# Performance work log

Measured on AMD Instinct MI355X. Metric: run time of the kernel, lower is better.

Reference implementation:

```python
import jax, jax.numpy as jnp
import numpy as np

N_ENTITY = 100000
N_RELATION = 32
DIM = 64
N_LAYER = 2
B = 4096
T = 32


def _knowledge_attention(h_set, path, t_emb, W1, W2):
    # h_set, path, t_emb: [B, T, D]
    x = jnp.concatenate([h_set, path], axis=-1)          # [B, T, 2D]
    a = jax.nn.sigmoid(jax.nn.sigmoid(x @ W1) @ W2)      # [B, T]
    w = jax.nn.softmax(a, axis=-1)                       # softmax over triples
    return jnp.einsum('bt,btd->bd', w, t_emb)            # [B, D]


def _branch(h_idx, r_idx, t_idx, ent, rel, W1, W2):
    # h_idx/r_idx/t_idx: [L, B, T] ints. Faithful to the original loop,
    # which re-adds layer-i head emb and re-multiplies layer-i relation emb i times.
    outs = []
    for i in range(N_LAYER):
        h_set = ent[h_idx[0]]                            # [B, T, D]
        path = rel[r_idx[0]]                             # [B, T, D]
        for _k in range(1, i + 1):
            h_set = h_set + ent[h_idx[i]]
            path = path * rel[r_idx[i]]
        outs.append(_knowledge_attention(h_set, path, ent[t_idx[i]], W1, W2))
    return outs


def setup_inputs() -> dict:
    key = jax.random.key(0)
    ks = jax.random.split(key, 20)
    d = {}
    d['items'] = jax.random.randint(ks[0], (B,), 0, N_ENTITY)
    names = ['uis', 'ipt', 'upt', 'iot']
    i = 1
    for nm in names:
        d[nm + '_h'] = jax.random.randint(ks[i], (N_LAYER, B, T), 0, N_ENTITY); i += 1
        d[nm + '_r'] = jax.random.randint(ks[i], (N_LAYER, B, T), 0, N_RELATION); i += 1
        d[nm + '_t'] = jax.random.randint(ks[i], (N_LAYER, B, T), 0, N_ENTITY); i += 1
    # xavier-ish scales
    d['ent_emb'] = jax.random.normal(ks[13], (N_ENTITY, DIM), jnp.float32) * 0.05
    d['rel_emb'] = jax.random.normal(ks[14], (N_RELATION, DIM), jnp.float32) * 0.05
    d['W1'] = jax.random.normal(ks[15], (2 * DIM, DIM), jnp.float32) * (1.0 / np.sqrt(2 * DIM))
    d['W2'] = jax.random.normal(ks[16], (DIM,), jnp.float32) * (1.0 / np.sqrt(DIM))
    return d


def reference(items, uis_h, uis_r, uis_t, ipt_h, ipt_r, ipt_t,
              upt_h, upt_r, upt_t, iot_h, iot_r, iot_t,
              ent_emb, rel_emb, W1, W2):
    # user embeddings (init triple set)
    user_embs = [ent_emb[uis_h[0]].mean(axis=1)]
    user_embs += _branch(uis_h, uis_r, uis_t, ent_emb, rel_emb, W1, W2)
    # item embeddings (potential triple set)
    item_embs = [ent_emb[items]]
    item_embs += _branch(ipt_h, ipt_r, ipt_t, ent_emb, rel_emb, W1, W2)
    # user potential embeddings
    upo_embs = [ent_emb[upt_h[0]].mean(axis=1)]
    upo_embs += _branch(upt_h, upt_r, upt_t, ent_emb, rel_emb, W1, W2)
    # item origin embeddings
    ior_embs = [ent_emb[iot_h[0]].mean(axis=1)]
    ior_embs += _branch(iot_h, iot_r, iot_t, ent_emb, rel_emb, W1, W2)
    # agg == 'sum': extra item term appended before predict
    item_embs.append(ent_emb[ipt_h[0]].mean(axis=1))
    e_u = sum(user_embs[1:], user_embs[0])
    e_i = sum(item_embs[1:], item_embs[0])
    e_p_u = sum(upo_embs[1:], upo_embs[0])
    e_p_i = sum(ior_embs[1:], ior_embs[0])
    e_u = jnp.concatenate([e_u, e_p_u], axis=-1)
    e_i = jnp.concatenate([e_p_i, e_i], axis=-1)
    scores = jax.nn.sigmoid((e_i * e_u).sum(axis=1))     # [B]
    kge_loss = jnp.float32(0.0)                          # agg='sum' path: no SSL loss
    return scores, kge_loss
```

## Files before the change

kernel.cpp:

```cpp
#include <hip/hip_runtime.h>


#define NE   100000
#define NR   32
#define DIMD 64
#define BB   4096
#define TT   32
#define BT   (BB * TT)

__device__ __forceinline__ float sigf(float x) { return 1.0f / (1.0f + __expf(-x)); }
__device__ __forceinline__ float4 ld4(const float* p) {
    return *reinterpret_cast<const float4*>(p);
}

__device__ __forceinline__ float b2f(unsigned short u) {
    return __builtin_bit_cast(float, ((unsigned)u) << 16);
}
__device__ __forceinline__ unsigned short f2b(float x) {
    unsigned b = __builtin_bit_cast(unsigned, x);
    b += 0x7FFF + ((b >> 16) & 1);
    return (unsigned short)(b >> 16);
}
__device__ __forceinline__ float4 u2f4(ushort4 v) {
    return make_float4(b2f(v.x), b2f(v.y), b2f(v.z), b2f(v.w));
}
__device__ __forceinline__ ushort4 ldu4(const unsigned short* p) {
    return *reinterpret_cast<const ushort4*>(p);
}

template <int CTRL>
__device__ __forceinline__ float dpp_add(float x) {
    int r = __builtin_amdgcn_update_dpp(0, __builtin_bit_cast(int, x), CTRL,
                                        0xf, 0xf, true);
    return x + __builtin_bit_cast(float, r);
}
__device__ __forceinline__ float reduce16(float x) {
    x = dpp_add<0x121>(x);
    x = dpp_add<0x122>(x);
    x = dpp_add<0x124>(x);
    x = dpp_add<0x128>(x);
    return x;
}

__global__ __launch_bounds__(256) void k_proj_ent(const float* __restrict__ ent,
                                                  const float* __restrict__ W1,
                                                  unsigned short* __restrict__ tab) {
    __shared__ float sR[64][68];
    const int tid = threadIdx.x;
    const int row0 = blockIdx.x * 64;

#pragma unroll
    for (int i = 0; i < 4; ++i) {
        const int idx = tid + 256 * i;
        const int r = idx >> 4;
        const int c = idx & 15;
        const int er = (row0 + r < NE) ? (row0 + r) : (NE - 1);
        const float4 rv = ld4(ent + er * DIMD + 4 * c);
        sR[r][4 * c + 0] = rv.x; sR[r][4 * c + 1] = rv.y;
        sR[r][4 * c + 2] = rv.z; sR[r][4 * c + 3] = rv.w;
    }
    __syncthreads();

    const int q = tid & 15;
    const int trow = tid >> 4;
    float4 acc0 = make_float4(0.f, 0.f, 0.f, 0.f);
    float4 acc1 = acc0, acc2 = acc0, acc3 = acc0;

#pragma unroll
    for (int kk = 0; kk < 16; ++kk) {
        const float4 r0 = ld4(&sR[4 * trow + 0][4 * kk]);
        const float4 r1 = ld4(&sR[4 * trow + 1][4 * kk]);
        const float4 r2 = ld4(&sR[4 * trow + 2][4 * kk]);
        const float4 r3 = ld4(&sR[4 * trow + 3][4 * kk]);
#pragma unroll
        for (int i = 0; i < 4; ++i) {
            const float4 wv = ld4(W1 + (4 * kk + i) * DIMD + 4 * q);
            const float s0 = (i == 0) ? r0.x : (i == 1) ? r0.y : (i == 2) ? r0.z : r0.w;
            const float s1 = (i == 0) ? r1.x : (i == 1) ? r1.y : (i == 2) ? r1.z : r1.w;
            const float s2 = (i == 0) ? r2.x : (i == 1) ? r2.y : (i == 2) ? r2.z : r2.w;
            const float s3 = (i == 0) ? r3.x : (i == 1) ? r3.y : (i == 2) ? r3.z : r3.w;
            acc0.x = fmaf(s0, wv.x, acc0.x); acc0.y = fmaf(s0, wv.y, acc0.y);
            acc0.z = fmaf(s0, wv.z, acc0.z); acc0.w = fmaf(s0, wv.w, acc0.w);
            acc1.x = fmaf(s1, wv.x, acc1.x); acc1.y = fmaf(s1, wv.y, acc1.y);
            acc1.z = fmaf(s1, wv.z, acc1.z); acc1.w = fmaf(s1, wv.w, acc1.w);
            acc2.x = fmaf(s2, wv.x, acc2.x); acc2.y = fmaf(s2, wv.y, acc2.y);
            acc2.z = fmaf(s2, wv.z, acc2.z); acc2.w = fmaf(s2, wv.w, acc2.w);
            acc3.x = fmaf(s3, wv.x, acc3.x); acc3.y = fmaf(s3, wv.y, acc3.y);
            acc3.z = fmaf(s3, wv.z, acc3.z); acc3.w = fmaf(s3, wv.w, acc3.w);
        }
    }

    const int orow = row0 + 4 * trow;
#pragma unroll
    for (int i = 0; i < 4; ++i) {
        if (orow + i < NE) {
            const float4 a = (i == 0) ? acc0 : (i == 1) ? acc1 : (i == 2) ? acc2 : acc3;
            unsigned short* rowp = tab + ((size_t)(orow + i) << 7);
            ushort4 ev, pv;
            ev.x = f2b(sR[4 * trow + i][4 * q + 0]);
            ev.y = f2b(sR[4 * trow + i][4 * q + 1]);
            ev.z = f2b(sR[4 * trow + i][4 * q + 2]);
            ev.w = f2b(sR[4 * trow + i][4 * q + 3]);
            pv.x = f2b(a.x); pv.y = f2b(a.y); pv.z = f2b(a.z); pv.w = f2b(a.w);
            *reinterpret_cast<ushort4*>(rowp + 4 * q) = ev;
            *reinterpret_cast<ushort4*>(rowp + 64 + 4 * q) = pv;
        }
    }
}

__global__ __launch_bounds__(256) void k_proj_rel(const float* __restrict__ rel,
                                                  const float* __restrict__ W1,
                                                  unsigned short* __restrict__ relB) {
    int gid = blockIdx.x * 256 + threadIdx.x;
    int row = gid >> 6;
    int d = gid & 63;
    if (row < 32) {
        const float* a = rel + row * DIMD;
        float acc = 0.0f;
#pragma unroll
        for (int k = 0; k < DIMD; ++k)
            acc = fmaf(a[k], W1[(DIMD + k) * DIMD + d], acc);
        relB[row * DIMD + d] = f2b(acc);
    } else if (row < 32 + 1024) {
        const int rr = row - 32;
        const float* a = rel + (rr >> 5) * DIMD;
        const float* c = rel + (rr & 31) * DIMD;
        float acc = 0.0f;
#pragma unroll
        for (int k = 0; k < DIMD; ++k)
            acc = fmaf(a[k] * c[k], W1[(DIMD + k) * DIMD + d], acc);
        relB[row * DIMD + d] = f2b(acc);
    }
}

__global__ __launch_bounds__(256) void k_main(
    const int* __restrict__ items,
    const int* __restrict__ uh, const int* __restrict__ ur, const int* __restrict__ ut,
    const int* __restrict__ ih, const int* __restrict__ ir, const int* __restrict__ itp,
    const int* __restrict__ ph, const int* __restrict__ pr, const int* __restrict__ pt,
    const int* __restrict__ oh, const int* __restrict__ orr, const int* __restrict__ ot,
    const unsigned short* __restrict__ tab,
    const unsigned short* __restrict__ relB,
    const float* __restrict__ W2,
    float* __restrict__ out) {
    const int b = blockIdx.x;
    const int tid = threadIdx.x;
    const int w = tid >> 6;
    const int lane = tid & 63;
    const int g = lane >> 4;
    const int q = lane & 15;

    const int* hp;
    const int* rp;
    const int* tp;
    switch (w) {
        case 0: hp = uh; rp = ur; tp = ut; break;
        case 1: hp = ih; rp = ir; tp = itp; break;
        case 2: hp = ph; rp = pr; tp = pt; break;
        default: hp = oh; rp = orr; tp = ot; break;
    }

    __shared__ int sidx[4][3][2][TT];
    {
        const int l = lane >> 5;
        const int t0 = lane & 31;
        const int off = l * BT + b * TT + t0;
        sidx[w][0][l][t0] = hp[off];
        sidx[w][1][l][t0] = rp[off];
        sidx[w][2][l][t0] = tp[off];
    }
    const int item_idx = (w == 1) ? items[b] : 0;

    int jh0[8], jh1[8], jr0[8], jr1[8], jt0[8], jt1[8];
#pragma unroll
    for (int p = 0; p < 8; ++p) {
        const int t = 4 * p + g;
        jh0[p] = sidx[w][0][0][t];
        jh1[p] = sidx[w][0][1][t];
        jr0[p] = sidx[w][1][0][t];
        jr1[p] = sidx[w][1][1][t];
        jt0[p] = sidx[w][2][0][t];
        jt1[p] = sidx[w][2][1][t];
    }

    ushort4 rH[8], rA0[8], rA1[8], rR0[8], rR2[8];
#pragma unroll
    for (int p = 0; p < 8; ++p) {
        const unsigned short* r0p = tab + ((size_t)jh0[p] << 7) + 4 * q;
        rH[p] = ldu4(r0p);
        rA0[p] = ldu4(r0p + 64);
        rA1[p] = ldu4(tab + ((size_t)jh1[p] << 7) + 64 + 4 * q);
        rR0[p] = ldu4(relB + ((size_t)jr0[p] << 6) + 4 * q);
        rR2[p] = ldu4(relB + ((size_t)(32 + jr0[p] * 32 + jr1[p]) << 6) + 4 * q);
    }

    const float4 w2v = ld4(W2 + 4 * q);

    float d0[8], d1[8];
    float4 accH = make_float4(0.f, 0.f, 0.f, 0.f);
#pragma unroll
    for (int p = 0; p < 8; ++p) {
        const float4 H = u2f4(rH[p]);
        const float4 A0 = u2f4(rA0[p]);
        const float4 A1 = u2f4(rA1[p]);
        const float4 R0 = u2f4(rR0[p]);
        const float4 R2 = u2f4(rR2[p]);

        accH.x += H.x; accH.y += H.y; accH.z += H.z; accH.w += H.w;

        float v = sigf(A0.x + R0.x) * w2v.x;
        v = fmaf(sigf(A0.y + R0.y), w2v.y, v);
        v = fmaf(sigf(A0.z + R0.z), w2v.z, v);
        v = fmaf(sigf(A0.w + R0.w), w2v.w, v);
        d0[p] = v;

        float u = sigf(A0.x + A1.x + R2.x) * w2v.x;
        u = fmaf(sigf(A0.y + A1.y + R2.y), w2v.y, u);
        u = fmaf(sigf(A0.z + A1.z + R2.z), w2v.z, u);
        u = fmaf(sigf(A0.w + A1.w + R2.w), w2v.w, u);
        d1[p] = u;
    }

    ushort4 rT0[8], rT1[8];
#pragma unroll
    for (int p = 0; p < 8; ++p) {
        rT0[p] = ldu4(tab + ((size_t)jt0[p] << 7) + 4 * q);
        rT1[p] = ldu4(tab + ((size_t)jt1[p] << 7) + 4 * q);
    }
    const ushort4 rIt = ldu4(tab + ((size_t)item_idx << 7) + 4 * q);

    float e0[8], e1[8];
    float s0 = 0.0f, s1 = 0.0f;
#pragma unroll
    for (int p = 0; p < 8; ++p) {
        e0[p] = __expf(sigf(reduce16(d0[p])));
        e1[p] = __expf(sigf(reduce16(d1[p])));
        s0 += e0[p];
        s1 += e1[p];
    }
    s0 += __shfl_xor(s0, 16, 64);
    s0 += __shfl_xor(s0, 32, 64);
    s1 += __shfl_xor(s1, 16, 64);
    s1 += __shfl_xor(s1, 32, 64);

    float4 acc0 = make_float4(0.f, 0.f, 0.f, 0.f);
    float4 acc1 = acc0;
#pragma unroll
    for (int p = 0; p < 8; ++p) {
        const float4 T0 = u2f4(rT0[p]);
        const float4 T1 = u2f4(rT1[p]);
        acc0.x = fmaf(e0[p], T0.x, acc0.x); acc0.y = fmaf(e0[p], T0.y, acc0.y);
        acc0.z = fmaf(e0[p], T0.z, acc0.z); acc0.w = fmaf(e0[p], T0.w, acc0.w);
        acc1.x = fmaf(e1[p], T1.x, acc1.x); acc1.y = fmaf(e1[p], T1.y, acc1.y);
        acc1.z = fmaf(e1[p], T1.z, acc1.z); acc1.w = fmaf(e1[p], T1.w, acc1.w);
    }

    const float inv0 = 1.0f / s0;
    const float inv1 = 1.0f / s1;
    float4 v;
    v.x = fmaf(acc0.x, inv0, fmaf(acc1.x, inv1, 0.03125f * accH.x));
    v.y = fmaf(acc0.y, inv0, fmaf(acc1.y, inv1, 0.03125f * accH.y));
    v.z = fmaf(acc0.z, inv0, fmaf(acc1.z, inv1, 0.03125f * accH.z));
    v.w = fmaf(acc0.w, inv0, fmaf(acc1.w, inv1, 0.03125f * accH.w));

    v.x += __shfl_xor(v.x, 16, 64); v.x += __shfl_xor(v.x, 32, 64);
    v.y += __shfl_xor(v.y, 16, 64); v.y += __shfl_xor(v.y, 32, 64);
    v.z += __shfl_xor(v.z, 16, 64); v.z += __shfl_xor(v.z, 32, 64);
    v.w += __shfl_xor(v.w, 16, 64); v.w += __shfl_xor(v.w, 32, 64);

    if (w == 1) {
        const float4 iv = u2f4(rIt);
        v.x += iv.x; v.y += iv.y; v.z += iv.z; v.w += iv.w;
    }

    __shared__ float vec[4][DIMD];
    if (g == 0) {
        vec[w][4 * q + 0] = v.x;
        vec[w][4 * q + 1] = v.y;
        vec[w][4 * q + 2] = v.z;
        vec[w][4 * q + 3] = v.w;
    }
    __syncthreads();

    if (tid < 64) {
        float z = fmaf(vec[0][tid], vec[3][tid], vec[2][tid] * vec[1][tid]);
#pragma unroll
        for (int m = 1; m < 64; m <<= 1) z += __shfl_xor(z, m, 64);
        if (tid == 0) out[b] = sigf(z);
    }
    if (b == 0 && tid == 0) out[BB] = 0.0f;
}

extern "C" void kernel_launch(void* const* d_in, const int* in_sizes, int n_in,
                              void* d_out, int out_size, void* d_ws, size_t ws_size,
                              hipStream_t stream) {
    const int* items = (const int*)d_in[0];
    const int* uh = (const int*)d_in[1];
    const int* ur = (const int*)d_in[2];
    const int* ut = (const int*)d_in[3];
    const int* ih = (const int*)d_in[4];
    const int* ir = (const int*)d_in[5];
    const int* itp = (const int*)d_in[6];
    const int* ph = (const int*)d_in[7];
    const int* pr = (const int*)d_in[8];
    const int* pt = (const int*)d_in[9];
    const int* oh = (const int*)d_in[10];
    const int* orr = (const int*)d_in[11];
    const int* ot = (const int*)d_in[12];
    const float* ent = (const float*)d_in[13];
    const float* rel = (const float*)d_in[14];
    const float* W1 = (const float*)d_in[15];
    const float* W2 = (const float*)d_in[16];
    float* out = (float*)d_out;

    unsigned short* relB = (unsigned short*)d_ws;
    unsigned short* tab = relB + 1056 * DIMD;

    hipLaunchKernelGGL(k_proj_ent, dim3((NE + 63) / 64), dim3(256), 0, stream,
                       ent, W1, tab);
    hipLaunchKernelGGL(k_proj_rel, dim3((1056 * 64 + 255) / 256), dim3(256), 0,
                       stream, rel, W1, relB);
    hipLaunchKernelGGL(k_main, dim3(BB), dim3(256), 0, stream, items, uh, ur, ut,
                       ih, ir, itp, ph, pr, pt, oh, orr, ot, tab, relB, W2, out);
}
```

Baseline: 202.4 us.

## Widen bf16 gathers to 16-byte loads with 8 lanes per row; stage W1 in LDS

The main kernel now assigns 8 lanes per embedding row instead of 16, so each lane gathers 8 bf16 values with one 16-byte load. It unpacks them with shift and mask, and each wave handles 8 triples per pass over 4 passes instead of 4 triples over 8. The per-triple reductions use 3 shuffle steps instead of 4 DPP steps, and the cross-group reductions gain one extra shuffle. Separately, the entity projection kernel stages W1 in shared memory instead of reading it from global memory inside the inner loop. This reduces load instruction count and gather transactions, but raises register pressure from the wider per-lane arrays.

```diff
diff --git a/kernel.cpp b/kernel.cpp
--- a/kernel.cpp
+++ b/kernel.cpp
@@ -13,38 +13,38 @@
     return *reinterpret_cast<const float4*>(p);
 }
 
-__device__ __forceinline__ float b2f(unsigned short u) {
-    return __builtin_bit_cast(float, ((unsigned)u) << 16);
-}
 __device__ __forceinline__ unsigned short f2b(float x) {
     unsigned b = __builtin_bit_cast(unsigned, x);
     b += 0x7FFF + ((b >> 16) & 1);
     return (unsigned short)(b >> 16);
 }
-__device__ __forceinline__ float4 u2f4(ushort4 v) {
-    return make_float4(b2f(v.x), b2f(v.y), b2f(v.z), b2f(v.w));
-}
-__device__ __forceinline__ ushort4 ldu4(const unsigned short* p) {
-    return *reinterpret_cast<const ushort4*>(p);
-}
-
-template <int CTRL>
-__device__ __forceinline__ float dpp_add(float x) {
-    int r = __builtin_amdgcn_update_dpp(0, __builtin_bit_cast(int, x), CTRL,
-                                        0xf, 0xf, true);
-    return x + __builtin_bit_cast(float, r);
-}
-__device__ __forceinline__ float reduce16(float x) {
-    x = dpp_add<0x121>(x);
-    x = dpp_add<0x122>(x);
-    x = dpp_add<0x124>(x);
-    x = dpp_add<0x128>(x);
+__device__ __forceinline__ float blo(unsigned u) {
+    return __builtin_bit_cast(float, u << 16);
+}
+__device__ __forceinline__ float bhi(unsigned u) {
+    return __builtin_bit_cast(float, u & 0xFFFF0000u);
+}
+__device__ __forceinline__ void unp8(uint4 v, float* f) {
+    f[0] = blo(v.x); f[1] = bhi(v.x);
+    f[2] = blo(v.y); f[3] = bhi(v.y);
+    f[4] = blo(v.z); f[5] = bhi(v.z);
+    f[6] = blo(v.w); f[7] = bhi(v.w);
+}
+__device__ __forceinline__ uint4 ldu4(const unsigned* p) {
+    return *reinterpret_cast<const uint4*>(p);
+}
+
+__device__ __forceinline__ float reduce8(float x) {
+    x += __shfl_xor(x, 1, 64);
+    x += __shfl_xor(x, 2, 64);
+    x += __shfl_xor(x, 4, 64);
     return x;
 }
 
 __global__ __launch_bounds__(256) void k_proj_ent(const float* __restrict__ ent,
                                                   const float* __restrict__ W1,
                                                   unsigned short* __restrict__ tab) {
+    __shared__ float sW[64][68];
     __shared__ float sR[64][68];
     const int tid = threadIdx.x;
     const int row0 = blockIdx.x * 64;
@@ -54,6 +54,9 @@
         const int idx = tid + 256 * i;
         const int r = idx >> 4;
         const int c = idx & 15;
+        const float4 wv = ld4(W1 + r * DIMD + 4 * c);
+        sW[r][4 * c + 0] = wv.x; sW[r][4 * c + 1] = wv.y;
+        sW[r][4 * c + 2] = wv.z; sW[r][4 * c + 3] = wv.w;
         const int er = (row0 + r < NE) ? (row0 + r) : (NE - 1);
         const float4 rv = ld4(ent + er * DIMD + 4 * c);
         sR[r][4 * c + 0] = rv.x; sR[r][4 * c + 1] = rv.y;
@@ -74,7 +77,7 @@
         const float4 r3 = ld4(&sR[4 * trow + 3][4 * kk]);
 #pragma unroll
         for (int i = 0; i < 4; ++i) {
-            const float4 wv = ld4(W1 + (4 * kk + i) * DIMD + 4 * q);
+            const float4 wv = ld4(&sW[4 * kk + i][4 * q]);
             const float s0 = (i == 0) ? r0.x : (i == 1) ? r0.y : (i == 2) ? r0.z : r0.w;
             const float s1 = (i == 0) ? r1.x : (i == 1) ? r1.y : (i == 2) ? r1.z : r1.w;
             const float s2 = (i == 0) ? r2.x : (i == 1) ? r2.y : (i == 2) ? r2.z : r2.w;
@@ -147,8 +150,8 @@
     const int tid = threadIdx.x;
     const int w = tid >> 6;
     const int lane = tid & 63;
-    const int g = lane >> 4;
-    const int q = lane & 15;
+    const int g = lane >> 3;
+    const int q = lane & 7;
 
     const int* hp;
     const int* rp;
@@ -171,10 +174,10 @@
     }
     const int item_idx = (w == 1) ? items[b] : 0;
 
-    int jh0[8], jh1[8], jr0[8], jr1[8], jt0[8], jt1[8];
-#pragma unroll
-    for (int p = 0; p < 8; ++p) {
-        const int t = 4 * p + g;
+    int jh0[4], jh1[4], jr0[4], jr1[4], jt0[4], jt1[4];
+#pragma unroll
+    for (int p = 0; p < 4; ++p) {
+        const int t = 8 * p + g;
         jh0[p] = sidx[w][0][0][t];
         jh1[p] = sidx[w][0][1][t];
         jr0[p] = sidx[w][1][0][t];
@@ -183,102 +186,109 @@
         jt1[p] = sidx[w][2][1][t];
     }
 
-    ushort4 rH[8], rA0[8], rA1[8], rR0[8], rR2[8];
-#pragma unroll
-    for (int p = 0; p < 8; ++p) {
-        const unsigned short* r0p = tab + ((size_t)jh0[p] << 7) + 4 * q;
+    const unsigned* tabU = (const unsigned*)tab;
+    const unsigned* relU = (const unsigned*)relB;
+
+    uint4 rH[4], rA0[4], rA1[4], rR0[4], rR2[4];
+#pragma unroll
+    for (int p = 0; p < 4; ++p) {
+        const unsigned* r0p = tabU + ((size_t)jh0[p] << 6) + 4 * q;
         rH[p] = ldu4(r0p);
-        rA0[p] = ldu4(r0p + 64);
-        rA1[p] = ldu4(tab + ((size_t)jh1[p] << 7) + 64 + 4 * q);
-        rR0[p] = ldu4(relB + ((size_t)jr0[p] << 6) + 4 * q);
-        rR2[p] = ldu4(relB + ((size_t)(32 + jr0[p] * 32 + jr1[p]) << 6) + 4 * q);
-    }
-
-    const float4 w2v = ld4(W2 + 4 * q);
-
-    float d0[8], d1[8];
-    float4 accH = make_float4(0.f, 0.f, 0.f, 0.f);
-#pragma unroll
-    for (int p = 0; p < 8; ++p) {
-        const float4 H = u2f4(rH[p]);
-        const float4 A0 = u2f4(rA0[p]);
-        const float4 A1 = u2f4(rA1[p]);
-        const float4 R0 = u2f4(rR0[p]);
-        const float4 R2 = u2f4(rR2[p]);
-
-        accH.x += H.x; accH.y += H.y; accH.z += H.z; accH.w += H.w;
-
-        float v = sigf(A0.x + R0.x) * w2v.x;
-        v = fmaf(sigf(A0.y + R0.y), w2v.y, v);
-        v = fmaf(sigf(A0.z + R0.z), w2v.z, v);
-        v = fmaf(sigf(A0.w + R0.w), w2v.w, v);
+        rA0[p] = ldu4(r0p + 32);
+        rA1[p] = ldu4(tabU + ((size_t)jh1[p] << 6) + 32 + 4 * q);
+        rR0[p] = ldu4(relU + ((size_t)jr0[p] << 5) + 4 * q);
+        rR2[p] = ldu4(relU + ((size_t)(32 + jr0[p] * 32 + jr1[p]) << 5) + 4 * q);
+    }
+
+    float w2e[8];
+    {
+        const float4 wa = ld4(W2 + 8 * q);
+        const float4 wb = ld4(W2 + 8 * q + 4);
+        w2e[0] = wa.x; w2e[1] = wa.y; w2e[2] = wa.z; w2e[3] = wa.w;
+        w2e[4] = wb.x; w2e[5] = wb.y; w2e[6] = wb.z; w2e[7] = wb.w;
+    }
+
+    float d0[4], d1[4];
+    float aH[8] = {0.f, 0.f, 0.f, 0.f, 0.f, 0.f, 0.f, 0.f};
+#pragma unroll
+    for (int p = 0; p < 4; ++p) {
+        float He[8], A0e[8], A1e[8], R0e[8], R2e[8];
+        unp8(rH[p], He);
+        unp8(rA0[p], A0e);
+        unp8(rA1[p], A1e);
+        unp8(rR0[p], R0e);
+        unp8(rR2[p], R2e);
+        float v = 0.f, u = 0.f;
+#pragma unroll
+        for (int j = 0; j < 8; ++j) {
+            aH[j] += He[j];
+            v = fmaf(sigf(A0e[j] + R0e[j]), w2e[j], v);
+            u = fmaf(sigf(A0e[j] + A1e[j] + R2e[j]), w2e[j], u);
+        }
         d0[p] = v;
-
-        float u = sigf(A0.x + A1.x + R2.x) * w2v.x;
-        u = fmaf(sigf(A0.y + A1.y + R2.y), w2v.y, u);
-        u = fmaf(sigf(A0.z + A1.z + R2.z), w2v.z, u);
-        u = fmaf(sigf(A0.w + A1.w + R2.w), w2v.w, u);
         d1[p] = u;
     }
 
-    ushort4 rT0[8], rT1[8];
-#pragma unroll
-    for (int p = 0; p < 8; ++p) {
-        rT0[p] = ldu4(tab + ((size_t)jt0[p] << 7) + 4 * q);
-        rT1[p] = ldu4(tab + ((size_t)jt1[p] << 7) + 4 * q);
-    }
-    const ushort4 rIt = ldu4(tab + ((size_t)item_idx << 7) + 4 * q);
-
-    float e0[8], e1[8];
-    float s0 = 0.0f, s1 = 0.0f;
-#pragma unroll
-    for (int p = 0; p < 8; ++p) {
-        e0[p] = __expf(sigf(reduce16(d0[p])));
-        e1[p] = __expf(sigf(reduce16(d1[p])));
+    uint4 rT0[4], rT1[4];
+#pragma unroll
+    for (int p = 0; p < 4; ++p) {
+        rT0[p] = ldu4(tabU + ((size_t)jt0[p] << 6) + 4 * q);
+        rT1[p] = ldu4(tabU + ((size_t)jt1[p] << 6) + 4 * q);
+    }
+    const uint4 rIt = ldu4(tabU + ((size_t)item_idx << 6) + 4 * q);
+
+    float e0[4], e1[4];
+    float s0 = 0.f, s1 = 0.f;
+#pragma unroll
+    for (int p = 0; p < 4; ++p) {
+        e0[p] = __expf(sigf(reduce8(d0[p])));
+        e1[p] = __expf(sigf(reduce8(d1[p])));
         s0 += e0[p];
         s1 += e1[p];
     }
+    s0 += __shfl_xor(s0, 8, 64);
     s0 += __shfl_xor(s0, 16, 64);
     s0 += __shfl_xor(s0, 32, 64);
+    s1 += __shfl_xor(s1, 8, 64);
     s1 += __shfl_xor(s1, 16, 64);
     s1 += __shfl_xor(s1, 32, 64);
 
-    float4 acc0 = make_float4(0.f, 0.f, 0.f, 0.f);
-    float4 acc1 = acc0;
-#pragma unroll
-    for (int p = 0; p < 8; ++p) {
-        const float4 T0 = u2f4(rT0[p]);
-        const float4 T1 = u2f4(rT1[p]);
-        acc0.x = fmaf(e0[p], T0.x, acc0.x); acc0.y = fmaf(e0[p], T0.y, acc0.y);
-        acc0.z = fmaf(e0[p], T0.z, acc0.z); acc0.w = fmaf(e0[p], T0.w, acc0.w);
-        acc1.x = fmaf(e1[p], T1.x, acc1.x); acc1.y = fmaf(e1[p], T1.y, acc1.y);
-        acc1.z = fmaf(e1[p], T1.z, acc1.z); acc1.w = fmaf(e1[p], T1.w, acc1.w);
+    float acc0[8] = {0.f, 0.f, 0.f, 0.f, 0.f, 0.f, 0.f, 0.f};
+    float acc1[8] = {0.f, 0.f, 0.f, 0.f, 0.f, 0.f, 0.f, 0.f};
+#pragma unroll
+    for (int p = 0; p < 4; ++p) {
+        float T0e[8], T1e[8];
+        unp8(rT0[p], T0e);
+        unp8(rT1[p], T1e);
+#pragma unroll
+        for (int j = 0; j < 8; ++j) {
+            acc0[j] = fmaf(e0[p], T0e[j], acc0[j]);
+            acc1[j] = fmaf(e1[p], T1e[j], acc1[j]);
+        }
     }
 
     const float inv0 = 1.0f / s0;
     const float inv1 = 1.0f / s1;
-    float4 v;
-    v.x = fmaf(acc0.x, inv0, fmaf(acc1.x, inv1, 0.03125f * accH.x));
-    v.y = fmaf(acc0.y, inv0, fmaf(acc1.y, inv1, 0.03125f * accH.y));
-    v.z = fmaf(acc0.z, inv0, fmaf(acc1.z, inv1, 0.03125f * accH.z));
-    v.w = fmaf(acc0.w, inv0, fmaf(acc1.w, inv1, 0.03125f * accH.w));
-
-    v.x += __shfl_xor(v.x, 16, 64); v.x += __shfl_xor(v.x, 32, 64);
-    v.y += __shfl_xor(v.y, 16, 64); v.y += __shfl_xor(v.y, 32, 64);
-    v.z += __shfl_xor(v.z, 16, 64); v.z += __shfl_xor(v.z, 32, 64);
-    v.w += __shfl_xor(v.w, 16, 64); v.w += __shfl_xor(v.w, 32, 64);
+    float ve[8];
+#pragma unroll
+    for (int j = 0; j < 8; ++j) {
+        ve[j] = fmaf(acc0[j], inv0, fmaf(acc1[j], inv1, 0.03125f * aH[j]));
+        ve[j] += __shfl_xor(ve[j], 8, 64);
+        ve[j] += __shfl_xor(ve[j], 16, 64);
+        ve[j] += __shfl_xor(ve[j], 32, 64);
+    }
 
     if (w == 1) {
-        const float4 iv = u2f4(rIt);
-        v.x += iv.x; v.y += iv.y; v.z += iv.z; v.w += iv.w;
+        float Ie[8];
+        unp8(rIt, Ie);
+#pragma unroll
+        for (int j = 0; j < 8; ++j) ve[j] += Ie[j];
     }
 
     __shared__ float vec[4][DIMD];
     if (g == 0) {
-        vec[w][4 * q + 0] = v.x;
-        vec[w][4 * q + 1] = v.y;
-        vec[w][4 * q + 2] = v.z;
-        vec[w][4 * q + 3] = v.w;
+#pragma unroll
+        for (int j = 0; j < 8; ++j) vec[w][8 * q + j] = ve[j];
     }
     __syncthreads();
 
```

After: 194.0 us. 4.1% less time.
